# Kernel tuning notes

Measured on AMD Instinct MI355X. Metric: run time of the kernel, lower is better.

Reference implementation:

```python
import jax, jax.numpy as jnp
import numpy as np

D, H, DH, L, DFF, V, K = 512, 8, 64, 6, 2048, 256, 5
N = 10240
TAU = 0.1
EPS = 1e-5


def _ln(x, w, b):
    m = x.mean(-1, keepdims=True)
    v = ((x - m) ** 2).mean(-1, keepdims=True)
    return (x - m) * jax.lax.rsqrt(v + EPS) * w + b


def _attn(q_in, kv_in, inw, inb, ow, ob):
    # q_in: [Q, D], kv_in: [M, D]; standard PyTorch MultiheadAttention math
    wq, wk, wv = jnp.split(inw, 3, 0)
    bq, bk, bv = jnp.split(inb, 3)
    q = (q_in @ wq.T + bq).reshape(-1, H, DH)
    k = (kv_in @ wk.T + bk).reshape(-1, H, DH)
    v = (kv_in @ wv.T + bv).reshape(-1, H, DH)
    s = jnp.einsum('qhd,mhd->hqm', q, k) / np.float32(np.sqrt(DH))
    o = jnp.einsum('hqm,mhd->qhd', jax.nn.softmax(s, -1), v).reshape(-1, D)
    return o @ ow.T + ob


def setup_inputs() -> dict:
    key = jax.random.key(0)
    ks = iter(jax.random.split(key, 64))

    def w(shape):
        return jax.random.normal(next(ks), shape, jnp.float32) * 0.02

    inp = {
        'input_bytes': jax.random.randint(next(ks), (N,), 0, V, jnp.int32),
        'emb': w((V, D)),
        'alpha': jnp.float32(0.5),
        'enc_inw': w((L, 3 * D, D)), 'enc_inb': w((L, 3 * D)),
        'enc_ow': w((L, D, D)), 'enc_ob': w((L, D)),
        'enc_w1': w((L, DFF, D)), 'enc_b1': w((L, DFF)),
        'enc_w2': w((L, D, DFF)), 'enc_b2': w((L, D)),
        'enc_ln1w': jnp.ones((L, D)), 'enc_ln1b': jnp.zeros((L, D)),
        'enc_ln2w': jnp.ones((L, D)), 'enc_ln2b': jnp.zeros((L, D)),
        'dec_sa_inw': w((L, 3 * D, D)), 'dec_sa_inb': w((L, 3 * D)),
        'dec_sa_ow': w((L, D, D)), 'dec_sa_ob': w((L, D)),
        'dec_ca_inw': w((L, 3 * D, D)), 'dec_ca_inb': w((L, 3 * D)),
        'dec_ca_ow': w((L, D, D)), 'dec_ca_ob': w((L, D)),
        'dec_w1': w((L, DFF, D)), 'dec_b1': w((L, DFF)),
        'dec_w2': w((L, D, DFF)), 'dec_b2': w((L, D)),
        'dec_ln1w': jnp.ones((L, D)), 'dec_ln1b': jnp.zeros((L, D)),
        'dec_ln2w': jnp.ones((L, D)), 'dec_ln2b': jnp.zeros((L, D)),
        'dec_ln3w': jnp.ones((L, D)), 'dec_ln3b': jnp.zeros((L, D)),
        'out_w': w((V, D)), 'out_b': w((V,)),
    }
    return inp


def reference(input_bytes, emb, alpha, enc_inw, enc_inb, enc_ow, enc_ob,
              enc_w1, enc_b1, enc_w2, enc_b2, enc_ln1w, enc_ln1b, enc_ln2w, enc_ln2b,
              dec_sa_inw, dec_sa_inb, dec_sa_ow, dec_sa_ob,
              dec_ca_inw, dec_ca_inb, dec_ca_ow, dec_ca_ob,
              dec_w1, dec_b1, dec_w2, dec_b2,
              dec_ln1w, dec_ln1b, dec_ln2w, dec_ln2b, dec_ln3w, dec_ln3b,
              out_w, out_b):
    P = input_bytes.shape[0] // K
    patches = input_bytes[:P * K].reshape(P, K)            # fixed k-byte patching
    x = emb[patches].mean(1)                               # mean-pooled patch embeddings [P, D]
    # ---- TransformerEncoder (post-LN, relu FFN, no dropout at eval) ----
    for l in range(L):
        x = _ln(x + _attn(x, x, enc_inw[l], enc_inb[l], enc_ow[l], enc_ob[l]), enc_ln1w[l], enc_ln1b[l])
        ff = jax.nn.relu(x @ enc_w1[l].T + enc_b1[l]) @ enc_w2[l].T + enc_b2[l]
        x = _ln(x + ff, enc_ln2w[l], enc_ln2b[l])
    encoded = x                                            # [P, D]
    # ---- gating + embedding mix (vectorized over the per-patch loop) ----
    gate = jnp.linalg.norm(encoded, axis=-1) > TAU
    tok = emb[patches[:, -1]]
    x = jnp.where(gate[:, None], alpha * encoded + (1.0 - alpha) * tok, tok)  # [P, D]
    # ---- TransformerDecoder: each patch is an independent length-1 target;
    #      self-attn over a single token reduces to out_proj(V(x));
    #      cross-attn attends to the full encoded memory (as in the original loop) ----
    for l in range(L):
        wv = dec_sa_inw[l][2 * D:]
        bv = dec_sa_inb[l][2 * D:]
        sa = (x @ wv.T + bv) @ dec_sa_ow[l].T + dec_sa_ob[l]
        x = _ln(x + sa, dec_ln1w[l], dec_ln1b[l])
        ca = _attn(x, encoded, dec_ca_inw[l], dec_ca_inb[l], dec_ca_ow[l], dec_ca_ob[l])
        x = _ln(x + ca, dec_ln2w[l], dec_ln2b[l])
        ff = jax.nn.relu(x @ dec_w1[l].T + dec_b1[l]) @ dec_w2[l].T + dec_b2[l]
        x = _ln(x + ff, dec_ln3w[l], dec_ln3b[l])
    return x @ out_w.T + out_b                             # [P, V]
```

## Files before the change

kernel.cpp:

```cpp
#include <hip/hip_runtime.h>
#include <hip/hip_bf16.h>
#include <math.h>

#define DD   512
#define HN   8
#define DHD  64
#define LL   6
#define DFF_ 2048
#define VV   256
#define KB_  5
#define PP   2048
#define EPS_ 1e-5f
#define TAU_ 0.1f
#define NS   4
#define KVS  (PP / NS)
#define QSCALE 0.18033688f
#define THRL2  11.5416f

typedef __attribute__((ext_vector_type(8))) short bf16x8;
typedef __attribute__((ext_vector_type(4))) short bf16x4;
typedef __attribute__((ext_vector_type(4))) float f32x4;

__device__ __forceinline__ float wave_sum(float v) {
#pragma unroll
  for (int m = 32; m >= 1; m >>= 1) v += __shfl_xor(v, m, 64);
  return v;
}

__device__ __forceinline__ unsigned short f2bf(float f) {
  unsigned u = __float_as_uint(f);
  u += 0x7FFF + ((u >> 16) & 1);
  return (unsigned short)(u >> 16);
}

__device__ __forceinline__ float bf2f(unsigned short u) {
  return __uint_as_float(((unsigned)u) << 16);
}

__device__ __forceinline__ bf16x8 cvt8(float4 a, float4 b) {
  bf16x8 v;
  v[0] = (short)f2bf(a.x); v[1] = (short)f2bf(a.y);
  v[2] = (short)f2bf(a.z); v[3] = (short)f2bf(a.w);
  v[4] = (short)f2bf(b.x); v[5] = (short)f2bf(b.y);
  v[6] = (short)f2bf(b.z); v[7] = (short)f2bf(b.w);
  return v;
}

__device__ __forceinline__ void gload16(const void* g, void* l) {
  __builtin_amdgcn_global_load_lds(
      (const __attribute__((address_space(1))) unsigned int*)g,
      (__attribute__((address_space(3))) unsigned int*)l, 16, 0, 0);
}

#define NSEG 55
struct CvtSeg { const float* src; short* dst; int n; };
struct CvtArgs { CvtSeg seg[NSEG]; };

__global__ __launch_bounds__(256) void convert_bf16_kernel(CvtArgs a) {
  const CvtSeg sg = a.seg[blockIdx.y];
  const int i = ((int)blockIdx.x * 256 + (int)threadIdx.x) * 16;
  if (i >= sg.n) return;
  const float4 x0 = *(const float4*)(sg.src + i);
  const float4 x1 = *(const float4*)(sg.src + i + 4);
  const float4 x2 = *(const float4*)(sg.src + i + 8);
  const float4 x3 = *(const float4*)(sg.src + i + 12);
  *(bf16x8*)(sg.dst + i)     = cvt8(x0, x1);
  *(bf16x8*)(sg.dst + i + 8) = cvt8(x2, x3);
}

__global__ __launch_bounds__(256) void transpose_wv_kernel(const float* __restrict__ sa_inw,
                                                           short* __restrict__ wvt) {
  __shared__ float t[64][65];
  const int l = blockIdx.z;
  const float* S = sa_inw + (size_t)l * 3 * DD * DD + (size_t)2 * DD * DD;
  short* D = wvt + (size_t)l * DD * DD;
  const int bo = blockIdx.y * 64;
  const int bi = blockIdx.x * 64;
  const int r = (int)threadIdx.x >> 2;
  const int c0 = ((int)threadIdx.x & 3) * 16;
#pragma unroll
  for (int j = 0; j < 16; j += 4)
    *(float4*)&t[r][c0 + j] = *(const float4*)&S[(size_t)(bo + r) * DD + bi + c0 + j];
  __syncthreads();
  bf16x8 o0, o1;
#pragma unroll
  for (int j = 0; j < 8; ++j) o0[j] = (short)f2bf(t[c0 + j][r]);
#pragma unroll
  for (int j = 0; j < 8; ++j) o1[j] = (short)f2bf(t[c0 + 8 + j][r]);
  short* dp = &D[(size_t)(bi + r) * DD + bo + c0];
  *(bf16x8*)dp = o0;
  *(bf16x8*)(dp + 8) = o1;
}

__global__ __launch_bounds__(256) void sa_bias_kernel(const float* __restrict__ sa_inb,
                                                      const float* __restrict__ sa_ow,
                                                      const float* __restrict__ sa_ob,
                                                      float* __restrict__ bc) {
  const int gid = (int)blockIdx.x * 4 + ((int)threadIdx.x >> 6);
  const int l = gid >> 9, n = gid & 511;
  const int lane = (int)threadIdx.x & 63;
  const float* wo = sa_ow + (size_t)l * DD * DD + (size_t)n * DD + lane * 8;
  const float* bv = sa_inb + (size_t)l * 3 * DD + 2 * DD + lane * 8;
  float s = 0.f;
#pragma unroll
  for (int j = 0; j < 8; ++j) s += wo[j] * bv[j];
  s = wave_sum(s);
  if (lane == 0) bc[(size_t)l * DD + n] = s + sa_ob[(size_t)l * DD + n];
}

__global__ __launch_bounds__(256) void gemm_wc_kernel(const short* __restrict__ WoBase,
                                                      size_t astr,
                                                      const short* __restrict__ WvT,
                                                      short* __restrict__ Wc) {
  constexpr int BK = 64;
  __shared__ short As[64 * BK];
  __shared__ short Bs[64 * BK];
  const int l = blockIdx.z;
  const short* A = WoBase + (size_t)l * astr;
  const short* W = WvT + (size_t)l * DD * DD;
  short* C = Wc + (size_t)l * DD * DD;
  const int tid = (int)threadIdx.x;
  const int lane = tid & 63;
  const int wid = tid >> 6;
  const int wm = (wid >> 1) * 32;
  const int wn = (wid & 1) * 32;
  const int bm = blockIdx.y * 64;
  const int bn = blockIdx.x * 64;
  const int fr = lane & 15;
  const int kq = lane >> 4;
  const int rs = fr & 7;
  const int srow = lane >> 3;
  const int scg = (lane & 7) ^ srow;

  f32x4 acc[2][2];
#pragma unroll
  for (int i = 0; i < 2; ++i)
#pragma unroll
    for (int j = 0; j < 2; ++j) acc[i][j] = (f32x4){0.f, 0.f, 0.f, 0.f};

  for (int k0 = 0; k0 < DD; k0 += BK) {
    __syncthreads();
#pragma unroll
    for (int is = 0; is < 2; ++is) {
      const int ib = is * 4 + wid;
      gload16(&A[(size_t)(bm + ib * 8 + srow) * DD + k0 + scg * 8], &As[ib * 512]);
      gload16(&W[(size_t)(bn + ib * 8 + srow) * DD + k0 + scg * 8], &Bs[ib * 512]);
    }
    __syncthreads();
#pragma unroll
    for (int s = 0; s < 2; ++s) {
      const int cg = s * 4 + kq;
      const int co = (cg ^ rs) * 8;
      bf16x8 af[2], bf[2];
#pragma unroll
      for (int i = 0; i < 2; ++i) af[i] = *(const bf16x8*)&As[(wm + i * 16 + fr) * BK + co];
#pragma unroll
      for (int j = 0; j < 2; ++j) bf[j] = *(const bf16x8*)&Bs[(wn + j * 16 + fr) * BK + co];
#pragma unroll
      for (int i = 0; i < 2; ++i)
#pragma unroll
        for (int j = 0; j < 2; ++j)
          acc[i][j] = __builtin_amdgcn_mfma_f32_16x16x32_bf16(af[i], bf[j], acc[i][j], 0, 0, 0);
    }
  }
  const int cr = (lane >> 4) * 4;
#pragma unroll
  for (int j = 0; j < 2; ++j) {
    const int col = bn + wn + j * 16 + fr;
#pragma unroll
    for (int i = 0; i < 2; ++i)
#pragma unroll
      for (int r = 0; r < 4; ++r)
        C[(size_t)(bm + wm + i * 16 + cr + r) * DD + col] = (short)f2bf(acc[i][j][r]);
  }
}

__global__ __launch_bounds__(256) void embed_mean_kernel(const int* __restrict__ bytes,
                                                         const float* __restrict__ emb,
                                                         short* __restrict__ xb,
                                                         float* __restrict__ tok) {
  const int p = blockIdx.x;
  const int d = threadIdx.x * 2;
  float a0 = 0.f, a1 = 0.f;
  int last = 0;
#pragma unroll
  for (int k = 0; k < KB_; ++k) {
    const int idx = bytes[p * KB_ + k];
    last = idx;
    const float* e = emb + (size_t)idx * DD + d;
    a0 += e[0]; a1 += e[1];
  }
  xb[(size_t)p * DD + d]     = (short)f2bf(a0 * 0.2f);
  xb[(size_t)p * DD + d + 1] = (short)f2bf(a1 * 0.2f);
  const float* e = emb + (size_t)last * DD + d;
  tok[(size_t)p * DD + d]     = e[0];
  tok[(size_t)p * DD + d + 1] = e[1];
}

template <int BM, int BN, int NSPLIT, int RELU, int WF32, int WBF16, int QS>
__global__ __launch_bounds__(256) void gemm_gl_kernel(
    const short* __restrict__ A, int lda,
    const short* __restrict__ W, int ldw,
    const float* __restrict__ bias,
    float* __restrict__ Cf, short* __restrict__ Cb, int ldc, int Kd,
    size_t pstride) {
  constexpr int BK = 128;
  __shared__ short As[BM * BK];
  __shared__ short Bs[BN * BK];
  constexpr int WM = BM / 2, WN = BN / 2;
  constexpr int MF = WM / 16, NF = WN / 16;
  const int tid = (int)threadIdx.x;
  const int lane = tid & 63;
  const int wid = tid >> 6;
  const int wm = (wid >> 1) * WM;
  const int wn = (wid & 1) * WN;
  const int bm = blockIdx.y * BM;
  const int bn = blockIdx.x * BN;
  const int fr = lane & 15;
  const int kq = lane >> 4;
  const int srow = lane >> 4;
  const int sc16 = lane & 15;

  const int kz = (NSPLIT > 1) ? (int)blockIdx.z : 0;
  const int kbeg = kz * (Kd / NSPLIT);
  const int kend = kbeg + Kd / NSPLIT;

  f32x4 acc[MF][NF];
#pragma unroll
  for (int i = 0; i < MF; ++i)
#pragma unroll
    for (int j = 0; j < NF; ++j) acc[i][j] = (f32x4){0.f, 0.f, 0.f, 0.f};

  for (int k0 = kbeg; k0 < kend; k0 += BK) {
    __syncthreads();
#pragma unroll
    for (int is = 0; is < BM / 16; ++is) {
      const int ib = is * 4 + wid;
      const int row = ib * 4 + srow;
      const int cg = sc16 ^ (row & 15);
      gload16(&A[(size_t)(bm + row) * lda + k0 + cg * 8], &As[ib * 512]);
    }
#pragma unroll
    for (int is = 0; is < BN / 16; ++is) {
      const int ib = is * 4 + wid;
      const int row = ib * 4 + srow;
      const int cg = sc16 ^ (row & 15);
      gload16(&W[(size_t)(bn + row) * ldw + k0 + cg * 8], &Bs[ib * 512]);
    }
    __syncthreads();
#pragma unroll
    for (int s = 0; s < 4; ++s) {
      const int co = ((s * 4 + kq) ^ fr) * 8;
      bf16x8 af[MF], bf[NF];
#pragma unroll
      for (int i = 0; i < MF; ++i)
        af[i] = *(const bf16x8*)&As[(wm + i * 16 + fr) * BK + co];
#pragma unroll
      for (int j = 0; j < NF; ++j)
        bf[j] = *(const bf16x8*)&Bs[(wn + j * 16 + fr) * BK + co];
#pragma unroll
      for (int i = 0; i < MF; ++i)
#pragma unroll
        for (int j = 0; j < NF; ++j)
          acc[i][j] = __builtin_amdgcn_mfma_f32_16x16x32_bf16(af[i], bf[j], acc[i][j], 0, 0, 0);
    }
  }

  const int cr = (lane >> 4) * 4;
  if constexpr (NSPLIT > 1) {
#pragma unroll
    for (int j = 0; j < NF; ++j) {
      const int col = bn + wn + j * 16 + fr;
#pragma unroll
      for (int i = 0; i < MF; ++i)
#pragma unroll
        for (int r = 0; r < 4; ++r) {
          const size_t idx = (size_t)(bm + wm + i * 16 + cr + r) * ldc + col;
          if (WF32) Cf[(size_t)kz * pstride + idx] = acc[i][j][r];
          else      Cb[(size_t)kz * pstride + idx] = (short)f2bf(acc[i][j][r]);
        }
    }
  } else {
#pragma unroll
    for (int j = 0; j < NF; ++j) {
      const int col = bn + wn + j * 16 + fr;
      const float bb = bias[col];
      const float sc = (QS && col < DD) ? QSCALE : 1.f;
#pragma unroll
      for (int i = 0; i < MF; ++i) {
#pragma unroll
        for (int r = 0; r < 4; ++r) {
          float v = (acc[i][j][r] + bb) * sc;
          if (RELU) v = fmaxf(v, 0.f);
          const size_t idx = (size_t)(bm + wm + i * 16 + cr + r) * ldc + col;
          if (WF32) Cf[idx] = v;
          if (WBF16) Cb[idx] = (short)f2bf(v);
        }
      }
    }
  }
}

__global__ __launch_bounds__(256) void gemm_ca_kernel(
    const short* __restrict__ Aq, const short* __restrict__ Akv,
    const short* __restrict__ Wfull, const float* __restrict__ bias,
    short* __restrict__ Cb) {
  constexpr int BK = 64;
  __shared__ short As[64 * BK];
  __shared__ short Bs[64 * BK];
  const int bx = (int)blockIdx.x;
  const int part_kv = bx >= 8;
  const short* A = part_kv ? Akv : Aq;
  const int wrow0 = part_kv ? DD + (bx - 8) * 64 : bx * 64;
  const float sc = part_kv ? 1.f : QSCALE;
  const int tid = (int)threadIdx.x;
  const int lane = tid & 63;
  const int wid = tid >> 6;
  const int wm = (wid >> 1) * 32;
  const int wn = (wid & 1) * 32;
  const int bm = blockIdx.y * 64;
  const int fr = lane & 15;
  const int kq = lane >> 4;
  const int rs = fr & 7;
  const int srow = lane >> 3;
  const int scg = (lane & 7) ^ srow;

  f32x4 acc[2][2];
#pragma unroll
  for (int i = 0; i < 2; ++i)
#pragma unroll
    for (int j = 0; j < 2; ++j) acc[i][j] = (f32x4){0.f, 0.f, 0.f, 0.f};

  for (int k0 = 0; k0 < DD; k0 += BK) {
    __syncthreads();
#pragma unroll
    for (int is = 0; is < 2; ++is) {
      const int ib = is * 4 + wid;
      gload16(&A[(size_t)(bm + ib * 8 + srow) * DD + k0 + scg * 8], &As[ib * 512]);
      gload16(&Wfull[(size_t)(wrow0 + ib * 8 + srow) * DD + k0 + scg * 8], &Bs[ib * 512]);
    }
    __syncthreads();
#pragma unroll
    for (int s = 0; s < 2; ++s) {
      const int cg = s * 4 + kq;
      const int co = (cg ^ rs) * 8;
      bf16x8 af[2], bf[2];
#pragma unroll
      for (int i = 0; i < 2; ++i) af[i] = *(const bf16x8*)&As[(wm + i * 16 + fr) * BK + co];
#pragma unroll
      for (int j = 0; j < 2; ++j) bf[j] = *(const bf16x8*)&Bs[(wn + j * 16 + fr) * BK + co];
#pragma unroll
      for (int i = 0; i < 2; ++i)
#pragma unroll
        for (int j = 0; j < 2; ++j)
          acc[i][j] = __builtin_amdgcn_mfma_f32_16x16x32_bf16(af[i], bf[j], acc[i][j], 0, 0, 0);
    }
  }
  const int cr = (lane >> 4) * 4;
#pragma unroll
  for (int j = 0; j < 2; ++j) {
    const int col = wrow0 + wn + j * 16 + fr;
    const float bb = bias[col];
#pragma unroll
    for (int i = 0; i < 2; ++i)
#pragma unroll
      for (int r = 0; r < 4; ++r)
        Cb[(size_t)(bm + wm + i * 16 + cr + r) * (3 * DD) + col] =
            (short)f2bf((acc[i][j][r] + bb) * sc);
  }
}

__global__ __launch_bounds__(256) void flash_attn_mfma_kernel(const short* __restrict__ qkvb,
                                                              short* __restrict__ Opart,
                                                              float* __restrict__ stats) {
  constexpr int LS = 72;
  __shared__ short Ks[64 * 64];
  __shared__ short Vt[64 * LS];
  __shared__ short Ps[64 * LS];
  const int h = blockIdx.y;
  const int q0 = blockIdx.x * 64;
  const int sp = blockIdx.z;
  const int tid = (int)threadIdx.x;
  const int lane = tid & 63;
  const int wid = tid >> 6;
  const int fr = lane & 15;
  const int g = lane >> 4;
  const int kg = g * 8;
  const int rs3 = fr & 7;

  bf16x8 qf[2];
  {
    const short* src = qkvb + (size_t)(q0 + wid * 16 + fr) * (3 * DD) + h * DHD + kg;
    qf[0] = *(const bf16x8*)src;
    qf[1] = *(const bf16x8*)(src + 32);
  }

  f32x4 acc_o[4];
#pragma unroll
  for (int df = 0; df < 4; ++df) acc_o[df] = (f32x4){0.f, 0.f, 0.f, 0.f};
  float mreg = -INFINITY, lsum = 0.f;

  const int srow8 = lane >> 3;
  const int sscg = (lane & 7) ^ srow8;
  const int vk2 = (tid & 31) * 2;
  const int vd8 = (tid >> 5) * 8;

  for (int t = 0; t < KVS / 64; ++t) {
    const int k0 = sp * KVS + t * 64;
    __syncthreads();
    {
#pragma unroll
      for (int p = 0; p < 2; ++p) {
        const int rb = p * 32 + wid * 8;
        gload16(&qkvb[(size_t)(k0 + rb + srow8) * (3 * DD) + DD + h * DHD + sscg * 8],
                &Ks[rb * 64]);
      }
      const short* vbase = qkvb + (size_t)(k0 + vk2) * (3 * DD) + 2 * DD + h * DHD + vd8;
      const bf16x8 v0 = *(const bf16x8*)vbase;
      const bf16x8 v1 = *(const bf16x8*)(vbase + 3 * DD);
#pragma unroll
      for (int j = 0; j < 8; ++j) {
        const unsigned pk = ((unsigned)(unsigned short)v0[j]) |
                            (((unsigned)(unsigned short)v1[j]) << 16);
        *(unsigned*)&Vt[(vd8 + j) * LS + vk2] = pk;
      }
    }
    __syncthreads();

    f32x4 st[4];
#pragma unroll
    for (int nf = 0; nf < 4; ++nf) st[nf] = (f32x4){0.f, 0.f, 0.f, 0.f};
    __builtin_amdgcn_s_setprio(1);
#pragma unroll
    for (int nf = 0; nf < 4; ++nf) {
      const int krow = (nf * 16 + fr) * 64;
      const bf16x8 kf0 = *(const bf16x8*)&Ks[krow + ((g ^ rs3) * 8)];
      const bf16x8 kf1 = *(const bf16x8*)&Ks[krow + (((g + 4) ^ rs3) * 8)];
      st[nf] = __builtin_amdgcn_mfma_f32_16x16x32_bf16(kf0, qf[0], st[nf], 0, 0, 0);
      st[nf] = __builtin_amdgcn_mfma_f32_16x16x32_bf16(kf1, qf[1], st[nf], 0, 0, 0);
    }
    __builtin_amdgcn_s_setprio(0);

    float mx = st[0][0];
#pragma unroll
    for (int nf = 0; nf < 4; ++nf)
#pragma unroll
      for (int i = 0; i < 4; ++i) mx = fmaxf(mx, st[nf][i]);
    mx = fmaxf(mx, __shfl_xor(mx, 16, 64));
    mx = fmaxf(mx, __shfl_xor(mx, 32, 64));

    if (!__all(mx <= mreg + THRL2)) {
      const float mn = fmaxf(mreg, mx);
      const float corr = exp2f(mreg - mn);
      mreg = mn;
      lsum *= corr;
      float corr_acc[4];
#pragma unroll
      for (int i = 0; i < 4; ++i)
        corr_acc[i] = __shfl(corr, (lane & 48) | (g * 4 + i), 64);
#pragma unroll
      for (int df = 0; df < 4; ++df) {
        acc_o[df][0] *= corr_acc[0]; acc_o[df][1] *= corr_acc[1];
        acc_o[df][2] *= corr_acc[2]; acc_o[df][3] *= corr_acc[3];
      }
    }

    float pv[4][4];
    float sum = 0.f;
#pragma unroll
    for (int nf = 0; nf < 4; ++nf)
#pragma unroll
      for (int i = 0; i < 4; ++i) {
        pv[nf][i] = exp2f(st[nf][i] - mreg);
        sum += pv[nf][i];
      }
    sum += __shfl_xor(sum, 16, 64);
    sum += __shfl_xor(sum, 32, 64);
    lsum += sum;

#pragma unroll
    for (int nf = 0; nf < 4; ++nf) {
      bf16x4 pw;
#pragma unroll
      for (int i = 0; i < 4; ++i) pw[i] = (short)f2bf(pv[nf][i]);
      *(bf16x4*)&Ps[(wid * 16 + fr) * LS + nf * 16 + g * 4] = pw;
    }
    asm volatile("s_waitcnt lgkmcnt(0)" ::: "memory");

    const bf16x8 pa0 = *(const bf16x8*)&Ps[(wid * 16 + fr) * LS + kg];
    const bf16x8 pa1 = *(const bf16x8*)&Ps[(wid * 16 + fr) * LS + kg + 32];
    __builtin_amdgcn_s_setprio(1);
#pragma unroll
    for (int df = 0; df < 4; ++df) {
      const bf16x8 vb0 = *(const bf16x8*)&Vt[(df * 16 + fr) * LS + kg];
      const bf16x8 vb1 = *(const bf16x8*)&Vt[(df * 16 + fr) * LS + kg + 32];
      acc_o[df] = __builtin_amdgcn_mfma_f32_16x16x32_bf16(pa0, vb0, acc_o[df], 0, 0, 0);
      acc_o[df] = __builtin_amdgcn_mfma_f32_16x16x32_bf16(pa1, vb1, acc_o[df], 0, 0, 0);
    }
    __builtin_amdgcn_s_setprio(0);
  }

  const int orow = q0 + wid * 16 + g * 4;
#pragma unroll
  for (int df = 0; df < 4; ++df)
#pragma unroll
    for (int i = 0; i < 4; ++i)
      Opart[((size_t)sp * PP + orow + i) * DD + h * DHD + df * 16 + fr] =
          (short)f2bf(acc_o[df][i]);
  if (g == 0) {
    const size_t si = (((size_t)sp * PP + q0 + wid * 16 + fr) * HN + h) * 2;
    stats[si]     = mreg;
    stats[si + 1] = lsum;
  }
}

__global__ __launch_bounds__(256) void attn_combine_kernel(const short* __restrict__ Opart,
                                                           const float* __restrict__ stats,
                                                           short* __restrict__ outb) {
  const int row = blockIdx.x * 4 + ((int)threadIdx.x >> 6);
  const int lane = (int)threadIdx.x & 63;
  const int d0 = lane * 8;
  const int h = d0 >> 6;
  float m[NS], l[NS];
  float M = -INFINITY;
#pragma unroll
  for (int s = 0; s < NS; ++s) {
    const size_t si = (((size_t)s * PP + row) * HN + h) * 2;
    m[s] = stats[si]; l[s] = stats[si + 1];
    M = fmaxf(M, m[s]);
  }
  float L = 0.f;
  float o[8];
#pragma unroll
  for (int j = 0; j < 8; ++j) o[j] = 0.f;
#pragma unroll
  for (int s = 0; s < NS; ++s) {
    const float e = exp2f(m[s] - M);
    L += l[s] * e;
    const bf16x8 v = *(const bf16x8*)&Opart[((size_t)s * PP + row) * DD + d0];
#pragma unroll
    for (int j = 0; j < 8; ++j) o[j] += bf2f((unsigned short)v[j]) * e;
  }
  const float inv = 1.f / L;
  bf16x8 ob;
#pragma unroll
  for (int j = 0; j < 8; ++j) ob[j] = (short)f2bf(o[j] * inv);
  *(bf16x8*)&outb[(size_t)row * DD + d0] = ob;
}

__global__ __launch_bounds__(256) void ln_residual_kernel(const short* __restrict__ xin,
                                                          const short* __restrict__ pA,
                                                          const short* __restrict__ pB,
                                                          const float* __restrict__ gb,
                                                          const float* __restrict__ w,
                                                          const float* __restrict__ b,
                                                          short* __restrict__ outb) {
  const int row = blockIdx.x * 4 + (threadIdx.x >> 6);
  const int lane = threadIdx.x & 63;
  const size_t base = (size_t)row * DD + lane * 8;
  float v[8];
  {
    const bf16x8 a = *(const bf16x8*)&xin[base];
    const bf16x8 r = *(const bf16x8*)&pA[base];
    const bf16x8 s = *(const bf16x8*)&pB[base];
    const float4 g0 = *(const float4*)&gb[lane * 8];
    const float4 g1 = *(const float4*)&gb[lane * 8 + 4];
    const float gg[8] = {g0.x, g0.y, g0.z, g0.w, g1.x, g1.y, g1.z, g1.w};
#pragma unroll
    for (int j = 0; j < 8; ++j)
      v[j] = bf2f((unsigned short)a[j]) + bf2f((unsigned short)r[j]) +
             bf2f((unsigned short)s[j]) + gg[j];
  }
  float sum = 0.f;
#pragma unroll
  for (int j = 0; j < 8; ++j) sum += v[j];
  sum = wave_sum(sum);
  const float mean = sum * (1.f / DD);
  float sq = 0.f;
#pragma unroll
  for (int j = 0; j < 8; ++j) { const float dd = v[j] - mean; sq += dd * dd; }
  sq = wave_sum(sq);
  const float rstd = rsqrtf(sq * (1.f / DD) + EPS_);
  const float* wp = w + lane * 8;
  const float* bp = b + lane * 8;
  bf16x8 ob;
#pragma unroll
  for (int j = 0; j < 8; ++j)
    ob[j] = (short)f2bf((v[j] - mean) * rstd * wp[j] + bp[j]);
  *(bf16x8*)&outb[base] = ob;
}

__global__ __launch_bounds__(256) void ln_gate_kernel(const short* __restrict__ xin,
                                                      const short* __restrict__ pA,
                                                      const short* __restrict__ pB,
                                                      const float* __restrict__ gb,
                                                      const float* __restrict__ w,
                                                      const float* __restrict__ b,
                                                      const float* __restrict__ tok,
                                                      const float* __restrict__ alpha_p,
                                                      short* __restrict__ xb,
                                                      short* __restrict__ encb) {
  const int row = blockIdx.x * 4 + (threadIdx.x >> 6);
  const int lane = threadIdx.x & 63;
  const size_t base = (size_t)row * DD + lane * 8;
  float v[8];
  {
    const bf16x8 a = *(const bf16x8*)&xin[base];
    const bf16x8 r = *(const bf16x8*)&pA[base];
    const bf16x8 s = *(const bf16x8*)&pB[base];
    const float4 g0 = *(const float4*)&gb[lane * 8];
    const float4 g1 = *(const float4*)&gb[lane * 8 + 4];
    const float gg[8] = {g0.x, g0.y, g0.z, g0.w, g1.x, g1.y, g1.z, g1.w};
#pragma unroll
    for (int j = 0; j < 8; ++j)
      v[j] = bf2f((unsigned short)a[j]) + bf2f((unsigned short)r[j]) +
             bf2f((unsigned short)s[j]) + gg[j];
  }
  float sum = 0.f;
#pragma unroll
  for (int j = 0; j < 8; ++j) sum += v[j];
  sum = wave_sum(sum);
  const float mean = sum * (1.f / DD);
  float sq = 0.f;
#pragma unroll
  for (int j = 0; j < 8; ++j) { const float dd = v[j] - mean; sq += dd * dd; }
  sq = wave_sum(sq);
  const float rstd = rsqrtf(sq * (1.f / DD) + EPS_);
  const float* wp = w + lane * 8;
  const float* bp = b + lane * 8;
  float e[8];
#pragma unroll
  for (int j = 0; j < 8; ++j) e[j] = (v[j] - mean) * rstd * wp[j] + bp[j];
  bf16x8 eb;
#pragma unroll
  for (int j = 0; j < 8; ++j) eb[j] = (short)f2bf(e[j]);
  *(bf16x8*)&encb[base] = eb;
  float nsq = 0.f;
#pragma unroll
  for (int j = 0; j < 8; ++j) nsq += e[j] * e[j];
  nsq = wave_sum(nsq);
  const bool gate = nsq > TAU_ * TAU_;
  const float a = *alpha_p;
  float t[8];
  {
    const float4 b0 = *(const float4*)&tok[base];
    const float4 b1 = *(const float4*)&tok[base + 4];
    t[0] = b0.x; t[1] = b0.y; t[2] = b0.z; t[3] = b0.w;
    t[4] = b1.x; t[5] = b1.y; t[6] = b1.z; t[7] = b1.w;
  }
  bf16x8 ob;
#pragma unroll
  for (int j = 0; j < 8; ++j)
    ob[j] = (short)f2bf(gate ? (a * e[j] + (1.f - a) * t[j]) : t[j]);
  *(bf16x8*)&xb[base] = ob;
}

__global__ __launch_bounds__(256) void out_combine_kernel(const float* __restrict__ P0,
                                                          const float* __restrict__ P1,
                                                          const float* __restrict__ bias,
                                                          float* __restrict__ out) {
  const size_t i = ((size_t)blockIdx.x * 256 + threadIdx.x) * 4;
  const int col = (int)(i % VV);
  const float4 a = *(const float4*)&P0[i];
  const float4 b = *(const float4*)&P1[i];
  const float4 c = *(const float4*)&bias[col];
  float4 o;
  o.x = a.x + b.x + c.x; o.y = a.y + b.y + c.y;
  o.z = a.z + b.z + c.z; o.w = a.w + b.w + c.w;
  *(float4*)&out[i] = o;
}

extern "C" void kernel_launch(void* const* d_in, const int* in_sizes, int n_in,
                              void* d_out, int out_size, void* d_ws, size_t ws_size,
                              hipStream_t stream) {
  const int*   bytes    = (const int*)d_in[0];
  const float* emb      = (const float*)d_in[1];
  const float* alpha    = (const float*)d_in[2];
  const float* enc_inw  = (const float*)d_in[3];
  const float* enc_inb  = (const float*)d_in[4];
  const float* enc_ow   = (const float*)d_in[5];
  const float* enc_ob   = (const float*)d_in[6];
  const float* enc_w1   = (const float*)d_in[7];
  const float* enc_b1   = (const float*)d_in[8];
  const float* enc_w2   = (const float*)d_in[9];
  const float* enc_b2   = (const float*)d_in[10];
  const float* enc_ln1w = (const float*)d_in[11];
  const float* enc_ln1b = (const float*)d_in[12];
  const float* enc_ln2w = (const float*)d_in[13];
  const float* enc_ln2b = (const float*)d_in[14];
  const float* dec_sa_inw = (const float*)d_in[15];
  const float* dec_sa_inb = (const float*)d_in[16];
  const float* dec_sa_ow  = (const float*)d_in[17];
  const float* dec_sa_ob  = (const float*)d_in[18];
  const float* dec_ca_inw = (const float*)d_in[19];
  const float* dec_ca_inb = (const float*)d_in[20];
  const float* dec_ca_ow  = (const float*)d_in[21];
  const float* dec_ca_ob  = (const float*)d_in[22];
  const float* dec_w1   = (const float*)d_in[23];
  const float* dec_b1   = (const float*)d_in[24];
  const float* dec_w2   = (const float*)d_in[25];
  const float* dec_b2   = (const float*)d_in[26];
  const float* dec_ln1w = (const float*)d_in[27];
  const float* dec_ln1b = (const float*)d_in[28];
  const float* dec_ln2w = (const float*)d_in[29];
  const float* dec_ln2b = (const float*)d_in[30];
  const float* dec_ln3w = (const float*)d_in[31];
  const float* dec_ln3b = (const float*)d_in[32];
  const float* out_w    = (const float*)d_in[33];
  const float* out_b    = (const float*)d_in[34];

  float* fp = (float*)d_ws;
  float* tok   = fp;  fp += (size_t)PP * DD;
  float* stats = fp;  fp += (size_t)NS * PP * HN * 2;
  float* outP  = fp;  fp += (size_t)2 * PP * VV;
  float* bcbuf = fp;  fp += (size_t)LL * DD;
  short* sp = (short*)fp;
  short* OpartB  = sp;  sp += (size_t)NS * PP * DD;
  short* tmpB    = sp;  sp += (size_t)2 * PP * DD;
  short* x_bf    = sp;  sp += (size_t)PP * DD;
  short* enc_bf  = sp;  sp += (size_t)PP * DD;
  short* qkv_bf  = sp;  sp += (size_t)PP * 3 * DD;
  short* attno_bf= sp;  sp += (size_t)PP * DD;
  short* ffh_bf  = sp;  sp += (size_t)PP * DFF_;
  short* wvT     = sp;  sp += (size_t)LL * DD * DD;
  short* wcM     = sp;  sp += (size_t)LL * DD * DD;
  short* warena  = sp;

  CvtArgs ca;
  size_t eoff[LL][4], doff[LL][5], ooff;
  size_t dec_start = 0, dec_stride = 0;
  {
    int si = 0;
    size_t off = 0;
    const size_t n0 = 3 * DD * DD, n1 = DD * DD, n2 = (size_t)DFF_ * DD, n3 = (size_t)DD * DFF_;
    for (int l = 0; l < LL; ++l) {
      ca.seg[si++] = {enc_inw + (size_t)l * n0, warena + off, (int)n0}; eoff[l][0] = off; off += n0;
      ca.seg[si++] = {enc_ow  + (size_t)l * n1, warena + off, (int)n1}; eoff[l][1] = off; off += n1;
      ca.seg[si++] = {enc_w1  + (size_t)l * n2, warena + off, (int)n2}; eoff[l][2] = off; off += n2;
      ca.seg[si++] = {enc_w2  + (size_t)l * n3, warena + off, (int)n3}; eoff[l][3] = off; off += n3;
    }
    dec_start = off;
    for (int l = 0; l < LL; ++l) {
      const size_t o0 = off;
      ca.seg[si++] = {dec_sa_ow  + (size_t)l * n1, warena + off, (int)n1}; doff[l][0] = off; off += n1;
      ca.seg[si++] = {dec_ca_inw + (size_t)l * n0, warena + off, (int)n0}; doff[l][1] = off; off += n0;
      ca.seg[si++] = {dec_ca_ow  + (size_t)l * n1, warena + off, (int)n1}; doff[l][2] = off; off += n1;
      ca.seg[si++] = {dec_w1     + (size_t)l * n2, warena + off, (int)n2}; doff[l][3] = off; off += n2;
      ca.seg[si++] = {dec_w2     + (size_t)l * n3, warena + off, (int)n3}; doff[l][4] = off; off += n3;
      if (l == 0) dec_stride = off - o0; (void)o0;
    }
    ca.seg[si++] = {out_w, warena + off, VV * DD}; ooff = off;
  }

  const dim3 b256(256);
  const dim3 gFA(PP / 64, HN, NS);
  const dim3 gQKV(3 * DD / 64, PP / 128);
  const dim3 gFF1(DFF_ / 64, PP / 128);
  const dim3 gS(DD / 64, PP / 64, 2);
  const dim3 gCA(24, PP / 64);
  const dim3 gOUTg(VV / 64, PP / 64, 2);
  const size_t psD = (size_t)PP * DD;
  const size_t psV = (size_t)PP * VV;

  convert_bf16_kernel<<<dim3(256, NSEG), b256, 0, stream>>>(ca);
  transpose_wv_kernel<<<dim3(8, 8, LL), b256, 0, stream>>>(dec_sa_inw, wvT);
  sa_bias_kernel<<<(LL * DD) / 4, b256, 0, stream>>>(dec_sa_inb, dec_sa_ow, dec_sa_ob, bcbuf);
  gemm_wc_kernel<<<dim3(8, 8, LL), b256, 0, stream>>>(warena + dec_start, dec_stride, wvT, wcM);
  embed_mean_kernel<<<PP, b256, 0, stream>>>(bytes, emb, x_bf, tok);

  for (int l = 0; l < LL; ++l) {
    const float* inb = enc_inb + (size_t)l * 3 * DD;
    const float* ob  = enc_ob  + (size_t)l * DD;
    const float* b1  = enc_b1  + (size_t)l * DFF_;
    const float* b2  = enc_b2  + (size_t)l * DD;

    gemm_gl_kernel<128, 64, 1, 0, 0, 1, 1><<<gQKV, b256, 0, stream>>>(
        x_bf, DD, warena + eoff[l][0], DD, inb, nullptr, qkv_bf, 3 * DD, DD, 0);
    flash_attn_mfma_kernel<<<gFA, b256, 0, stream>>>(qkv_bf, OpartB, stats);
    attn_combine_kernel<<<PP / 4, b256, 0, stream>>>(OpartB, stats, attno_bf);
    gemm_gl_kernel<64, 64, 2, 0, 0, 0, 0><<<gS, b256, 0, stream>>>(
        attno_bf, DD, warena + eoff[l][1], DD, nullptr, nullptr, tmpB, DD, DD, psD);
    ln_residual_kernel<<<PP / 4, b256, 0, stream>>>(
        x_bf, tmpB, tmpB + psD, ob, enc_ln1w + (size_t)l * DD, enc_ln1b + (size_t)l * DD, x_bf);
    gemm_gl_kernel<128, 64, 1, 1, 0, 1, 0><<<gFF1, b256, 0, stream>>>(
        x_bf, DD, warena + eoff[l][2], DD, b1, nullptr, ffh_bf, DFF_, DD, 0);
    gemm_gl_kernel<64, 64, 2, 0, 0, 0, 0><<<gS, b256, 0, stream>>>(
        ffh_bf, DFF_, warena + eoff[l][3], DFF_, nullptr, nullptr, tmpB, DD, DFF_, psD);
    if (l + 1 < LL) {
      ln_residual_kernel<<<PP / 4, b256, 0, stream>>>(
          x_bf, tmpB, tmpB + psD, b2, enc_ln2w + (size_t)l * DD, enc_ln2b + (size_t)l * DD, x_bf);
    } else {
      ln_gate_kernel<<<PP / 4, b256, 0, stream>>>(
          x_bf, tmpB, tmpB + psD, b2, enc_ln2w + (size_t)l * DD, enc_ln2b + (size_t)l * DD,
          tok, alpha, x_bf, enc_bf);
    }
  }

  for (int l = 0; l < LL; ++l) {
    const float* ca_inb = dec_ca_inb + (size_t)l * 3 * DD;
    const float* ca_ob  = dec_ca_ob + (size_t)l * DD;
    const float* b1 = dec_b1 + (size_t)l * DFF_;
    const float* b2 = dec_b2 + (size_t)l * DD;

    gemm_gl_kernel<64, 64, 2, 0, 0, 0, 0><<<gS, b256, 0, stream>>>(
        x_bf, DD, wcM + (size_t)l * DD * DD, DD, nullptr, nullptr, tmpB, DD, DD, psD);
    ln_residual_kernel<<<PP / 4, b256, 0, stream>>>(
        x_bf, tmpB, tmpB + psD, bcbuf + (size_t)l * DD,
        dec_ln1w + (size_t)l * DD, dec_ln1b + (size_t)l * DD, x_bf);

    gemm_ca_kernel<<<gCA, b256, 0, stream>>>(
        x_bf, enc_bf, warena + doff[l][1], ca_inb, qkv_bf);
    flash_attn_mfma_kernel<<<gFA, b256, 0, stream>>>(qkv_bf, OpartB, stats);
    attn_combine_kernel<<<PP / 4, b256, 0, stream>>>(OpartB, stats, attno_bf);
    gemm_gl_kernel<64, 64, 2, 0, 0, 0, 0><<<gS, b256, 0, stream>>>(
        attno_bf, DD, warena + doff[l][2], DD, nullptr, nullptr, tmpB, DD, DD, psD);
    ln_residual_kernel<<<PP / 4, b256, 0, stream>>>(
        x_bf, tmpB, tmpB + psD, ca_ob, dec_ln2w + (size_t)l * DD, dec_ln2b + (size_t)l * DD, x_bf);

    gemm_gl_kernel<128, 64, 1, 1, 0, 1, 0><<<gFF1, b256, 0, stream>>>(
        x_bf, DD, warena + doff[l][3], DD, b1, nullptr, ffh_bf, DFF_, DD, 0);
    gemm_gl_kernel<64, 64, 2, 0, 0, 0, 0><<<gS, b256, 0, stream>>>(
        ffh_bf, DFF_, warena + doff[l][4], DFF_, nullptr, nullptr, tmpB, DD, DFF_, psD);
    ln_residual_kernel<<<PP / 4, b256, 0, stream>>>(
        x_bf, tmpB, tmpB + psD, b2, dec_ln3w + (size_t)l * DD, dec_ln3b + (size_t)l * DD, x_bf);
  }

  gemm_gl_kernel<64, 64, 2, 0, 1, 0, 0><<<gOUTg, b256, 0, stream>>>(
      x_bf, DD, warena + ooff, DD, nullptr, outP, nullptr, VV, DD, psV);
  out_combine_kernel<<<(PP * VV / 4) / 256, b256, 0, stream>>>(
      outP, outP + psV, out_b, (float*)d_out);
}
```

Before: 981.4 us.

## Raise split-K factor to four and widen cross-attn GEMM K tile

The split-K factor for the D-output GEMMs (attention out-proj, FFN2, decoder self-attn, output head) goes from two to four. This launches more workgroups to fill the GPU's compute units, and the LayerNorm and output-combine kernels now sum four partial buffers through a strided loop. Separately, the cross-attention QKV GEMM moves to a 128-wide K tile with a 16-way XOR swizzle, which halves the number of barrier-separated load iterations. The cost is twice as much partial-sum traffic to write and read back, plus more shared memory per block in the CA GEMM.

```diff
diff --git a/kernel.cpp b/kernel.cpp
--- a/kernel.cpp
+++ b/kernel.cpp
@@ -14,6 +14,7 @@
 #define TAU_ 0.1f
 #define NS   4
 #define KVS  (PP / NS)
+#define KSP  4
 #define QSCALE 0.18033688f
 #define THRL2  11.5416f
 
@@ -305,7 +306,7 @@
     const short* __restrict__ Aq, const short* __restrict__ Akv,
     const short* __restrict__ Wfull, const float* __restrict__ bias,
     short* __restrict__ Cb) {
-  constexpr int BK = 64;
+  constexpr int BK = 128;
   __shared__ short As[64 * BK];
   __shared__ short Bs[64 * BK];
   const int bx = (int)blockIdx.x;
@@ -321,9 +322,8 @@
   const int bm = blockIdx.y * 64;
   const int fr = lane & 15;
   const int kq = lane >> 4;
-  const int rs = fr & 7;
-  const int srow = lane >> 3;
-  const int scg = (lane & 7) ^ srow;
+  const int srow = lane >> 4;
+  const int sc16 = lane & 15;
 
   f32x4 acc[2][2];
 #pragma unroll
@@ -334,16 +334,23 @@
   for (int k0 = 0; k0 < DD; k0 += BK) {
     __syncthreads();
 #pragma unroll
-    for (int is = 0; is < 2; ++is) {
+    for (int is = 0; is < 4; ++is) {
       const int ib = is * 4 + wid;
-      gload16(&A[(size_t)(bm + ib * 8 + srow) * DD + k0 + scg * 8], &As[ib * 512]);
-      gload16(&Wfull[(size_t)(wrow0 + ib * 8 + srow) * DD + k0 + scg * 8], &Bs[ib * 512]);
+      const int row = ib * 4 + srow;
+      const int cg = sc16 ^ (row & 15);
+      gload16(&A[(size_t)(bm + row) * DD + k0 + cg * 8], &As[ib * 512]);
+    }
+#pragma unroll
+    for (int is = 0; is < 4; ++is) {
+      const int ib = is * 4 + wid;
+      const int row = ib * 4 + srow;
+      const int cg = sc16 ^ (row & 15);
+      gload16(&Wfull[(size_t)(wrow0 + row) * DD + k0 + cg * 8], &Bs[ib * 512]);
     }
     __syncthreads();
 #pragma unroll
-    for (int s = 0; s < 2; ++s) {
-      const int cg = s * 4 + kq;
-      const int co = (cg ^ rs) * 8;
+    for (int s = 0; s < 4; ++s) {
+      const int co = ((s * 4 + kq) ^ fr) * 8;
       bf16x8 af[2], bf[2];
 #pragma unroll
       for (int i = 0; i < 2; ++i) af[i] = *(const bf16x8*)&As[(wm + i * 16 + fr) * BK + co];
@@ -549,8 +556,8 @@
 }
 
 __global__ __launch_bounds__(256) void ln_residual_kernel(const short* __restrict__ xin,
-                                                          const short* __restrict__ pA,
-                                                          const short* __restrict__ pB,
+                                                          const short* __restrict__ pP,
+                                                          size_t pstride,
                                                           const float* __restrict__ gb,
                                                           const float* __restrict__ w,
                                                           const float* __restrict__ b,
@@ -561,15 +568,17 @@
   float v[8];
   {
     const bf16x8 a = *(const bf16x8*)&xin[base];
-    const bf16x8 r = *(const bf16x8*)&pA[base];
-    const bf16x8 s = *(const bf16x8*)&pB[base];
     const float4 g0 = *(const float4*)&gb[lane * 8];
     const float4 g1 = *(const float4*)&gb[lane * 8 + 4];
     const float gg[8] = {g0.x, g0.y, g0.z, g0.w, g1.x, g1.y, g1.z, g1.w};
 #pragma unroll
-    for (int j = 0; j < 8; ++j)
-      v[j] = bf2f((unsigned short)a[j]) + bf2f((unsigned short)r[j]) +
-             bf2f((unsigned short)s[j]) + gg[j];
+    for (int j = 0; j < 8; ++j) v[j] = bf2f((unsigned short)a[j]) + gg[j];
+#pragma unroll
+    for (int s = 0; s < KSP; ++s) {
+      const bf16x8 p = *(const bf16x8*)&pP[s * pstride + base];
+#pragma unroll
+      for (int j = 0; j < 8; ++j) v[j] += bf2f((unsigned short)p[j]);
+    }
   }
   float sum = 0.f;
 #pragma unroll
@@ -591,8 +600,8 @@
 }
 
 __global__ __launch_bounds__(256) void ln_gate_kernel(const short* __restrict__ xin,
-                                                      const short* __restrict__ pA,
-                                                      const short* __restrict__ pB,
+                                                      const short* __restrict__ pP,
+                                                      size_t pstride,
                                                       const float* __restrict__ gb,
                                                       const float* __restrict__ w,
                                                       const float* __restrict__ b,
@@ -606,15 +615,17 @@
   float v[8];
   {
     const bf16x8 a = *(const bf16x8*)&xin[base];
-    const bf16x8 r = *(const bf16x8*)&pA[base];
-    const bf16x8 s = *(const bf16x8*)&pB[base];
     const float4 g0 = *(const float4*)&gb[lane * 8];
     const float4 g1 = *(const float4*)&gb[lane * 8 + 4];
     const float gg[8] = {g0.x, g0.y, g0.z, g0.w, g1.x, g1.y, g1.z, g1.w};
 #pragma unroll
-    for (int j = 0; j < 8; ++j)
-      v[j] = bf2f((unsigned short)a[j]) + bf2f((unsigned short)r[j]) +
-             bf2f((unsigned short)s[j]) + gg[j];
+    for (int j = 0; j < 8; ++j) v[j] = bf2f((unsigned short)a[j]) + gg[j];
+#pragma unroll
+    for (int s = 0; s < KSP; ++s) {
+      const bf16x8 p = *(const bf16x8*)&pP[s * pstride + base];
+#pragma unroll
+      for (int j = 0; j < 8; ++j) v[j] += bf2f((unsigned short)p[j]);
+    }
   }
   float sum = 0.f;
 #pragma unroll
@@ -655,18 +666,19 @@
   *(bf16x8*)&xb[base] = ob;
 }
 
-__global__ __launch_bounds__(256) void out_combine_kernel(const float* __restrict__ P0,
-                                                          const float* __restrict__ P1,
+__global__ __launch_bounds__(256) void out_combine_kernel(const float* __restrict__ P,
+                                                          size_t pstride,
                                                           const float* __restrict__ bias,
                                                           float* __restrict__ out) {
   const size_t i = ((size_t)blockIdx.x * 256 + threadIdx.x) * 4;
   const int col = (int)(i % VV);
-  const float4 a = *(const float4*)&P0[i];
-  const float4 b = *(const float4*)&P1[i];
   const float4 c = *(const float4*)&bias[col];
-  float4 o;
-  o.x = a.x + b.x + c.x; o.y = a.y + b.y + c.y;
-  o.z = a.z + b.z + c.z; o.w = a.w + b.w + c.w;
+  float4 o = c;
+#pragma unroll
+  for (int s = 0; s < KSP; ++s) {
+    const float4 a = *(const float4*)&P[s * pstride + i];
+    o.x += a.x; o.y += a.y; o.z += a.z; o.w += a.w;
+  }
   *(float4*)&out[i] = o;
 }
 
@@ -712,11 +724,11 @@
   float* fp = (float*)d_ws;
   float* tok   = fp;  fp += (size_t)PP * DD;
   float* stats = fp;  fp += (size_t)NS * PP * HN * 2;
-  float* outP  = fp;  fp += (size_t)2 * PP * VV;
+  float* outP  = fp;  fp += (size_t)KSP * PP * VV;
   float* bcbuf = fp;  fp += (size_t)LL * DD;
   short* sp = (short*)fp;
   short* OpartB  = sp;  sp += (size_t)NS * PP * DD;
-  short* tmpB    = sp;  sp += (size_t)2 * PP * DD;
+  short* tmpB    = sp;  sp += (size_t)KSP * PP * DD;
   short* x_bf    = sp;  sp += (size_t)PP * DD;
   short* enc_bf  = sp;  sp += (size_t)PP * DD;
   short* qkv_bf  = sp;  sp += (size_t)PP * 3 * DD;
@@ -756,9 +768,9 @@
   const dim3 gFA(PP / 64, HN, NS);
   const dim3 gQKV(3 * DD / 64, PP / 128);
   const dim3 gFF1(DFF_ / 64, PP / 128);
-  const dim3 gS(DD / 64, PP / 64, 2);
+  const dim3 gS(DD / 64, PP / 64, KSP);
   const dim3 gCA(24, PP / 64);
-  const dim3 gOUTg(VV / 64, PP / 64, 2);
+  const dim3 gOUTg(VV / 64, PP / 64, KSP);
   const size_t psD = (size_t)PP * DD;
   const size_t psV = (size_t)PP * VV;
 
@@ -778,20 +790,20 @@
         x_bf, DD, warena + eoff[l][0], DD, inb, nullptr, qkv_bf, 3 * DD, DD, 0);
     flash_attn_mfma_kernel<<<gFA, b256, 0, stream>>>(qkv_bf, OpartB, stats);
     attn_combine_kernel<<<PP / 4, b256, 0, stream>>>(OpartB, stats, attno_bf);
-    gemm_gl_kernel<64, 64, 2, 0, 0, 0, 0><<<gS, b256, 0, stream>>>(
+    gemm_gl_kernel<64, 64, KSP, 0, 0, 0, 0><<<gS, b256, 0, stream>>>(
         attno_bf, DD, warena + eoff[l][1], DD, nullptr, nullptr, tmpB, DD, DD, psD);
     ln_residual_kernel<<<PP / 4, b256, 0, stream>>>(
-        x_bf, tmpB, tmpB + psD, ob, enc_ln1w + (size_t)l * DD, enc_ln1b + (size_t)l * DD, x_bf);
+        x_bf, tmpB, psD, ob, enc_ln1w + (size_t)l * DD, enc_ln1b + (size_t)l * DD, x_bf);
     gemm_gl_kernel<128, 64, 1, 1, 0, 1, 0><<<gFF1, b256, 0, stream>>>(
         x_bf, DD, warena + eoff[l][2], DD, b1, nullptr, ffh_bf, DFF_, DD, 0);
-    gemm_gl_kernel<64, 64, 2, 0, 0, 0, 0><<<gS, b256, 0, stream>>>(
+    gemm_gl_kernel<64, 64, KSP, 0, 0, 0, 0><<<gS, b256, 0, stream>>>(
         ffh_bf, DFF_, warena + eoff[l][3], DFF_, nullptr, nullptr, tmpB, DD, DFF_, psD);
     if (l + 1 < LL) {
       ln_residual_kernel<<<PP / 4, b256, 0, stream>>>(
-          x_bf, tmpB, tmpB + psD, b2, enc_ln2w + (size_t)l * DD, enc_ln2b + (size_t)l * DD, x_bf);
+          x_bf, tmpB, psD, b2, enc_ln2w + (size_t)l * DD, enc_ln2b + (size_t)l * DD, x_bf);
     } else {
       ln_gate_kernel<<<PP / 4, b256, 0, stream>>>(
-          x_bf, tmpB, tmpB + psD, b2, enc_ln2w + (size_t)l * DD, enc_ln2b + (size_t)l * DD,
+          x_bf, tmpB, psD, b2, enc_ln2w + (size_t)l * DD, enc_ln2b + (size_t)l * DD,
           tok, alpha, x_bf, enc_bf);
     }
   }
@@ -802,31 +814,31 @@
     const float* b1 = dec_b1 + (size_t)l * DFF_;
     const float* b2 = dec_b2 + (size_t)l * DD;
 
-    gemm_gl_kernel<64, 64, 2, 0, 0, 0, 0><<<gS, b256, 0, stream>>>(
+    gemm_gl_kernel<64, 64, KSP, 0, 0, 0, 0><<<gS, b256, 0, stream>>>(
         x_bf, DD, wcM + (size_t)l * DD * DD, DD, nullptr, nullptr, tmpB, DD, DD, psD);
     ln_residual_kernel<<<PP / 4, b256, 0, stream>>>(
-        x_bf, tmpB, tmpB + psD, bcbuf + (size_t)l * DD,
+        x_bf, tmpB, psD, bcbuf + (size_t)l * DD,
         dec_ln1w + (size_t)l * DD, dec_ln1b + (size_t)l * DD, x_bf);
 
     gemm_ca_kernel<<<gCA, b256, 0, stream>>>(
         x_bf, enc_bf, warena + doff[l][1], ca_inb, qkv_bf);
     flash_attn_mfma_kernel<<<gFA, b256, 0, stream>>>(qkv_bf, OpartB, stats);
     attn_combine_kernel<<<PP / 4, b256, 0, stream>>>(OpartB, stats, attno_bf);
-    gemm_gl_kernel<64, 64, 2, 0, 0, 0, 0><<<gS, b256, 0, stream>>>(
+    gemm_gl_kernel<64, 64, KSP, 0, 0, 0, 0><<<gS, b256, 0, stream>>>(
         attno_bf, DD, warena + doff[l][2], DD, nullptr, nullptr, tmpB, DD, DD, psD);
     ln_residual_kernel<<<PP / 4, b256, 0, stream>>>(
-        x_bf, tmpB, tmpB + psD, ca_ob, dec_ln2w + (size_t)l * DD, dec_ln2b + (size_t)l * DD, x_bf);
+        x_bf, tmpB, psD, ca_ob, dec_ln2w + (size_t)l * DD, dec_ln2b + (size_t)l * DD, x_bf);
 
     gemm_gl_kernel<128, 64, 1, 1, 0, 1, 0><<<gFF1, b256, 0, stream>>>(
         x_bf, DD, warena + doff[l][3], DD, b1, nullptr, ffh_bf, DFF_, DD, 0);
-    gemm_gl_kernel<64, 64, 2, 0, 0, 0, 0><<<gS, b256, 0, stream>>>(
+    gemm_gl_kernel<64, 64, KSP, 0, 0, 0, 0><<<gS, b256, 0, stream>>>(
         ffh_bf, DFF_, warena + doff[l][4], DFF_, nullptr, nullptr, tmpB, DD, DFF_, psD);
     ln_residual_kernel<<<PP / 4, b256, 0, stream>>>(
-        x_bf, tmpB, tmpB + psD, b2, dec_ln3w + (size_t)l * DD, dec_ln3b + (size_t)l * DD, x_bf);
-  }
-
-  gemm_gl_kernel<64, 64, 2, 0, 1, 0, 0><<<gOUTg, b256, 0, stream>>>(
+        x_bf, tmpB, psD, b2, dec_ln3w + (size_t)l * DD, dec_ln3b + (size_t)l * DD, x_bf);
+  }
+
+  gemm_gl_kernel<64, 64, KSP, 0, 1, 0, 0><<<gOUTg, b256, 0, stream>>>(
       x_bf, DD, warena + ooff, DD, nullptr, outP, nullptr, VV, DD, psV);
   out_combine_kernel<<<(PP * VV / 4) / 256, b256, 0, stream>>>(
-      outP, outP + psV, out_b, (float*)d_out);
-}
+      outP, psV, out_b, (float*)d_out);
+}
```

After: 1.038 ms. 1.06x slower.
